# Kernel tuning notes

Measured on AMD Instinct MI355X. Metric: run time of the kernel, lower is better.

The kernel has to match this reference:

```python
import jax, jax.numpy as jnp
import numpy as np

EPS = 1e-5  # torch LayerNorm default
B, P, E, H = 16, 2048, 768, 256


def setup_inputs() -> dict:
    key = jax.random.key(0)
    k_x, k_qkv, k_lw = jax.random.split(key, 3)
    return {
        "x": jax.random.normal(k_x, (B, P, E), dtype=jnp.float32),
        "norm_w": jnp.ones((P, E), dtype=jnp.float32),
        "norm_b": jnp.zeros((P, E), dtype=jnp.float32),
        "qkv_w": jax.random.normal(k_qkv, (E, 3 * H), dtype=jnp.float32) * 0.02,
        "lin_w": jax.random.normal(k_lw, (E, H), dtype=jnp.float32) * 0.02,
        "lin_b": jnp.zeros((E,), dtype=jnp.float32),
    }


def reference(x, norm_w, norm_b, qkv_w, lin_w, lin_b):
    # LayerNorm over the last TWO dims (P, E) jointly, per batch element
    mean = jnp.mean(x, axis=(1, 2), keepdims=True)
    var = jnp.var(x, axis=(1, 2), keepdims=True)
    xn = (x - mean) * jax.lax.rsqrt(var + EPS) * norm_w + norm_b

    # QKV projection: [B,P,E] @ [E,3H] -> [B,P,3H]
    qkv = jnp.einsum("bpe,eh->bph", xn, qkv_w)
    q, k, v = jnp.split(qkv, 3, axis=2)  # each [B,P,H]

    # Unnormalized attention (no scale, no softmax)
    atten = jnp.einsum("bpd,bqd->bpq", q, k)  # [B,P,P]
    o = jnp.einsum("bpq,bqd->bpd", atten, v)  # [B,P,H]

    # Dropout p=0.0 (eval) -> identity; then Linear(H -> E) + ReLU
    out = jnp.einsum("bph,eh->bpe", o, lin_w) + lin_b
    return jax.nn.relu(out)
```

## Files before the change

kernel.cpp:

```cpp
#include <hip/hip_runtime.h>
#include <cstdint>

typedef unsigned short u16;
typedef __bf16 bf16x8 __attribute__((ext_vector_type(8)));
typedef float floatx4 __attribute__((ext_vector_type(4)));

#define BB 16
#define PP 2048
#define EE 768
#define HH 256
#define PE (PP * EE)
#define MM (BB * PP)

__device__ __forceinline__ u16 f2bf(float f) {
  union { float f; uint32_t u; } v; v.f = f;
  return (u16)((v.u + 0x7fffu + ((v.u >> 16) & 1u)) >> 16);
}

__device__ __forceinline__ void gload16(const void* g, void* l) {
  typedef __attribute__((address_space(1))) const void GV;
  typedef __attribute__((address_space(3))) void LV;
  __builtin_amdgcn_global_load_lds((GV*)g, (LV*)l, 16, 0, 0);
}

__device__ __forceinline__ int xcd_remap(int orig, int nwg) {
  return (orig & 7) * (nwg >> 3) + (orig >> 3);
}

__device__ __forceinline__ void zero_acc(floatx4 acc[4][4]) {
  const floatx4 z = {0.f, 0.f, 0.f, 0.f};
#pragma unroll
  for (int i = 0; i < 4; ++i)
#pragma unroll
    for (int j = 0; j < 4; ++j) acc[i][j] = z;
}

__device__ __forceinline__ void gemm_core(const u16* A, int lda, const u16* B, int ldb,
                                          int kIters, u16* As, u16* Bs,
                                          floatx4 acc[4][4]) {
  const int tid  = threadIdx.x;
  const int lane = tid & 63;
  const int wr   = (tid >> 7) & 1;
  const int wc   = (tid >> 6) & 1;
  const int srow = tid >> 3;
  const int scol = (tid & 7) << 3;
  const int mrow = lane & 15;
  const int kgrp = (lane >> 4) << 3;
  for (int kk = 0; kk < kIters; ++kk) {
    const u16* Ak = A + kk * 64;
    const u16* Bk = B + kk * 64;
    __syncthreads();
#pragma unroll
    for (int r = 0; r < 4; ++r) {
      gload16(Ak + (size_t)(r * 32 + srow) * lda + scol, (char*)As + r * 4096 + tid * 16);
      gload16(Bk + (size_t)(r * 32 + srow) * ldb + scol, (char*)Bs + r * 4096 + tid * 16);
    }
    __syncthreads();
#pragma unroll
    for (int kp = 0; kp < 2; ++kp) {
      const int ko = kp * 32 + kgrp;
      bf16x8 af[4], bq[4];
#pragma unroll
      for (int i = 0; i < 4; ++i) {
        af[i] = *(const bf16x8*)(As + (wr * 64 + i * 16 + mrow) * 64 + ko);
        bq[i] = *(const bf16x8*)(Bs + (wc * 64 + i * 16 + mrow) * 64 + ko);
      }
#pragma unroll
      for (int i = 0; i < 4; ++i)
#pragma unroll
        for (int j = 0; j < 4; ++j)
          acc[i][j] = __builtin_amdgcn_mfma_f32_16x16x32_bf16(af[i], bq[j], acc[i][j], 0, 0, 0);
    }
  }
}

template <typename F>
__device__ __forceinline__ void epilogue(floatx4 acc[4][4], F f) {
  const int lane = threadIdx.x & 63;
  const int wr = (threadIdx.x >> 7) & 1, wc = (threadIdx.x >> 6) & 1;
  const int r0 = (lane >> 4) * 4, c0 = lane & 15;
#pragma unroll
  for (int i = 0; i < 4; ++i)
#pragma unroll
    for (int j = 0; j < 4; ++j)
#pragma unroll
      for (int r = 0; r < 4; ++r)
        f(wr * 64 + i * 16 + r0 + r, wc * 64 + j * 16 + c0, acc[i][j][r]);
}

__global__ __launch_bounds__(256) void k_reduce1(const float* __restrict__ x,
                                                 float* __restrict__ psum,
                                                 float* __restrict__ psq) {
  const int b = blockIdx.y, blk = blockIdx.x, tid = threadIdx.x;
  const float4* xb = (const float4*)(x + (size_t)b * PE + (size_t)blk * 12288);
  float s = 0.f, q = 0.f;
#pragma unroll
  for (int i = 0; i < 12; ++i) {
    float4 v = xb[tid + i * 256];
    s += v.x + v.y + v.z + v.w;
    q += v.x * v.x + v.y * v.y + v.z * v.z + v.w * v.w;
  }
  for (int off = 32; off > 0; off >>= 1) { s += __shfl_down(s, off); q += __shfl_down(q, off); }
  __shared__ float ls[4], lq[4];
  if ((tid & 63) == 0) { ls[tid >> 6] = s; lq[tid >> 6] = q; }
  __syncthreads();
  if (tid == 0) {
    psum[b * 128 + blk] = ls[0] + ls[1] + ls[2] + ls[3];
    psq [b * 128 + blk] = lq[0] + lq[1] + lq[2] + lq[3];
  }
}

__global__ void k_reduce2(const float* __restrict__ psum, const float* __restrict__ psq,
                          float* __restrict__ stats) {
  const int b = blockIdx.x, tid = threadIdx.x;
  float s = psum[b * 128 + tid], q = psq[b * 128 + tid];
  for (int off = 32; off > 0; off >>= 1) { s += __shfl_down(s, off); q += __shfl_down(q, off); }
  __shared__ float ls[2], lq[2];
  if ((tid & 63) == 0) { ls[tid >> 6] = s; lq[tid >> 6] = q; }
  __syncthreads();
  if (tid == 0) {
    float S = ls[0] + ls[1], Q = lq[0] + lq[1];
    const float invN = 1.f / (float)PE;
    float mean = S * invN;
    float var = Q * invN - mean * mean;
    stats[b * 2] = mean;
    stats[b * 2 + 1] = rsqrtf(var + 1e-5f);
  }
}

__global__ __launch_bounds__(256) void k_ln(const float* __restrict__ x,
                                            const float* __restrict__ w,
                                            const float* __restrict__ bia,
                                            const float* __restrict__ stats,
                                            u16* __restrict__ xn) {
  const float4* x4 = (const float4*)x;
  const float4* w4 = (const float4*)w;
  const float4* b4 = (const float4*)bia;
  for (int vi = blockIdx.x * 256 + threadIdx.x; vi < (PE / 4) * BB; vi += gridDim.x * 256) {
    int bidx = vi / (PE / 4);
    int wi = vi - bidx * (PE / 4);
    float4 xv = x4[vi], wv = w4[wi], bv = b4[wi];
    float mean = stats[bidx * 2], rstd = stats[bidx * 2 + 1];
    ushort4 o;
    o.x = f2bf((xv.x - mean) * rstd * wv.x + bv.x);
    o.y = f2bf((xv.y - mean) * rstd * wv.y + bv.y);
    o.z = f2bf((xv.z - mean) * rstd * wv.z + bv.z);
    o.w = f2bf((xv.w - mean) * rstd * wv.w + bv.w);
    ((ushort4*)xn)[vi] = o;
  }
}

__global__ void k_transpose_w(const float* __restrict__ src, u16* __restrict__ dst) {
  __shared__ float t[32][33];
  const int e0 = blockIdx.x * 32, n0 = blockIdx.y * 32;
  const int tx = threadIdx.x, ty = threadIdx.y;
#pragma unroll
  for (int j = 0; j < 4; ++j)
    t[ty + j * 8][tx] = src[(size_t)(e0 + ty + j * 8) * 768 + n0 + tx];
  __syncthreads();
#pragma unroll
  for (int j = 0; j < 4; ++j)
    dst[(size_t)(n0 + ty + j * 8) * 768 + e0 + tx] = f2bf(t[tx][ty + j * 8]);
}

__global__ void k_cast(const float* __restrict__ src, u16* __restrict__ dst, int n4) {
  int i = blockIdx.x * 256 + threadIdx.x;
  if (i < n4) {
    float4 v = ((const float4*)src)[i];
    ushort4 o;
    o.x = f2bf(v.x); o.y = f2bf(v.y); o.z = f2bf(v.z); o.w = f2bf(v.w);
    ((ushort4*)dst)[i] = o;
  }
}

__global__ __launch_bounds__(256) void k_gemm_qkv(const u16* __restrict__ xn,
                                                  const u16* __restrict__ wT,
                                                  u16* __restrict__ q_buf,
                                                  u16* __restrict__ kT,
                                                  u16* __restrict__ vT) {
  __shared__ __align__(16) u16 sbuf[128 * 64 * 2];
  u16* As = sbuf;
  u16* Bs = sbuf + 128 * 64;
  floatx4 acc[4][4];
  zero_acc(acc);
  const int t = xcd_remap(blockIdx.x, 1536);
  const int xt = t % 6, yt = t / 6;
  const int tM = yt * 128, tN = xt * 128;
  gemm_core(xn + (size_t)tM * EE, EE, wT + (size_t)tN * EE, EE, 12, As, Bs, acc);

  if (xt < 2) {
    epilogue(acc, [&](int gr, int gc, float v) {
      q_buf[(size_t)(tM + gr) * HH + xt * 128 + gc] = f2bf(v);
    });
  } else {
    const int b = yt >> 4;
    const int p_base = (yt & 15) * 128;
    u16* dst = ((xt < 4) ? kT : vT) + (size_t)b * (HH * PP);
    const int dbase = (xt - ((xt < 4) ? 2 : 4)) * 128;
    u16 (*tt)[144] = (u16(*)[144])sbuf;
    const int tid = threadIdx.x;
    const int lane = tid & 63;
    const int wr = (tid >> 7) & 1, wc = (tid >> 6) & 1;
    const int r0 = (lane >> 4) * 4, c0 = lane & 15;
#pragma unroll
    for (int h = 0; h < 2; ++h) {
      __syncthreads();
      if (wc == h) {
#pragma unroll
        for (int i = 0; i < 4; ++i)
#pragma unroll
          for (int j = 0; j < 4; ++j)
#pragma unroll
            for (int r = 0; r < 4; ++r)
              tt[j * 16 + c0][wr * 64 + i * 16 + r0 + r] = f2bf(acc[i][j][r]);
      }
      __syncthreads();
#pragma unroll
      for (int pass = 0; pass < 4; ++pass) {
        const int row = pass * 16 + (tid >> 4);
        const int p8 = (tid & 15) * 8;
        const int d = dbase + h * 64 + row;
        uint4 vdat = *(const uint4*)&tt[row][p8];
        *(uint4*)&dst[(size_t)d * PP + p_base + p8] = vdat;
      }
    }
  }
}

__global__ __launch_bounds__(256) void k_gemm_w2(const u16* __restrict__ kT,
                                                 const u16* __restrict__ vT,
                                                 float* __restrict__ part) {
  __shared__ __align__(16) u16 As[128 * 64], Bs[128 * 64];
  floatx4 acc[4][4];
  zero_acc(acc);
  const int t = xcd_remap(blockIdx.x, 512);
  const int xt = t & 1, yt = (t >> 1) & 1, z = t >> 2;
  const int b = z >> 3, s = z & 7;
  const int tM = yt * 128, tN = xt * 128;
  const u16* A = kT + (size_t)b * (HH * PP) + (size_t)tM * PP + s * 256;
  const u16* B = vT + (size_t)b * (HH * PP) + (size_t)tN * PP + s * 256;
  gemm_core(A, PP, B, PP, 4, As, Bs, acc);
  float* P = part + (size_t)z * 65536;
  epilogue(acc, [&](int gr, int gc, float v) {
    P[(size_t)(tM + gr) * 256 + tN + gc] = v;
  });
}

__global__ void k_reduce_w2(const float* __restrict__ part, u16* __restrict__ W2) {
  const int idx = blockIdx.x * 256 + threadIdx.x;
  const int b = idx >> 16, i = idx & 65535;
  const float* p = part + ((size_t)b << 19) + i;
  float s = 0.f;
#pragma unroll
  for (int t = 0; t < 8; ++t) s += p[(size_t)t << 16];
  W2[idx] = f2bf(s);
}

__global__ __launch_bounds__(256) void k_gemm_m2(const u16* __restrict__ lwB,
                                                 const u16* __restrict__ W2,
                                                 u16* __restrict__ M2T) {
  __shared__ __align__(16) u16 As[128 * 64], Bs[128 * 64];
  floatx4 acc[4][4];
  zero_acc(acc);
  const int t = xcd_remap(blockIdx.x, 192);
  const int xt = t & 1, yt = (t >> 1) % 6, b = t / 12;
  const int tM = yt * 128, tN = xt * 128;
  const u16* A = lwB + (size_t)tM * HH;
  const u16* B = W2 + (size_t)b * 65536 + (size_t)tN * HH;
  gemm_core(A, HH, B, HH, 4, As, Bs, acc);
  u16* Mb = M2T + (size_t)b * (EE * HH);
  epilogue(acc, [&](int gr, int gc, float v) {
    Mb[(size_t)(tM + gr) * HH + tN + gc] = f2bf(v);
  });
}

__global__ __launch_bounds__(256) void k_gemm_out(const u16* __restrict__ q_buf,
                                                  const u16* __restrict__ M2T,
                                                  const float* __restrict__ lb,
                                                  float* __restrict__ out) {
  __shared__ __align__(16) u16 As[128 * 64], Bs[128 * 64];
  floatx4 acc[4][4];
  zero_acc(acc);
  const int t = xcd_remap(blockIdx.x, 1536);
  const int xt = t % 6, yt = (t / 6) % 16, b = t / 96;
  const int tM = yt * 128, tN = xt * 128;
  const u16* A = q_buf + (size_t)b * (PP * HH) + (size_t)tM * HH;
  const u16* B = M2T + (size_t)b * (EE * HH) + (size_t)tN * HH;
  gemm_core(A, HH, B, HH, 4, As, Bs, acc);
  float* ob = out + (size_t)b * PE;
  epilogue(acc, [&](int gr, int gc, float v) {
    ob[(size_t)(tM + gr) * EE + tN + gc] = fmaxf(v + lb[tN + gc], 0.f);
  });
}

extern "C" void kernel_launch(void* const* d_in, const int* in_sizes, int n_in,
                              void* d_out, int out_size, void* d_ws, size_t ws_size,
                              hipStream_t stream) {
  (void)in_sizes; (void)n_in; (void)out_size;
  const float* x  = (const float*)d_in[0];
  const float* nw = (const float*)d_in[1];
  const float* nb = (const float*)d_in[2];
  const float* qw = (const float*)d_in[3];
  const float* lw = (const float*)d_in[4];
  const float* lb = (const float*)d_in[5];
  float* out = (float*)d_out;
  char* ws = (char*)d_ws;

  size_t off = 0;
  auto alloc = [&](size_t bytes) { size_t o = off; off += (bytes + 255) & ~(size_t)255; return o; };
  const size_t o_psum = alloc(16 * 128 * 4);
  const size_t o_psq  = alloc(16 * 128 * 4);
  const size_t o_st   = alloc(16 * 2 * 4);
  const size_t o_qwT  = alloc((size_t)768 * 768 * 2);
  const size_t o_lwB  = alloc((size_t)768 * 256 * 2);
  const size_t o_q    = alloc((size_t)MM * HH * 2);
  const size_t o_kT   = alloc((size_t)BB * HH * PP * 2);
  const size_t o_vT   = alloc((size_t)BB * HH * PP * 2);
  const size_t o_W2   = alloc((size_t)BB * HH * HH * 2);
  const size_t o_M2T  = alloc((size_t)BB * EE * HH * 2);
  const size_t need_base = off;
  const size_t region = (size_t)MM * EE * 2;

  char* big = (ws_size >= need_base + region) ? (ws + need_base) : (char*)d_out;

  float* psum = (float*)(ws + o_psum);
  float* psq  = (float*)(ws + o_psq);
  float* st   = (float*)(ws + o_st);
  u16* qwT    = (u16*)(ws + o_qwT);
  u16* lwB    = (u16*)(ws + o_lwB);
  u16* q_buf  = (u16*)(ws + o_q);
  u16* kT     = (u16*)(ws + o_kT);
  u16* vT     = (u16*)(ws + o_vT);
  u16* W2     = (u16*)(ws + o_W2);
  u16* M2T    = (u16*)(ws + o_M2T);
  u16* xn     = (u16*)big;
  float* part = (float*)big;

  k_reduce1<<<dim3(128, 16), 256, 0, stream>>>(x, psum, psq);
  k_reduce2<<<16, 128, 0, stream>>>(psum, psq, st);
  k_ln<<<2048, 256, 0, stream>>>(x, nw, nb, st, xn);
  k_transpose_w<<<dim3(24, 24), dim3(32, 8), 0, stream>>>(qw, qwT);
  k_cast<<<192, 256, 0, stream>>>(lw, lwB, 768 * 256 / 4);
  k_gemm_qkv<<<1536, 256, 0, stream>>>(xn, qwT, q_buf, kT, vT);
  k_gemm_w2<<<512, 256, 0, stream>>>(kT, vT, part);
  k_reduce_w2<<<4096, 256, 0, stream>>>(part, W2);
  k_gemm_m2<<<192, 256, 0, stream>>>(lwB, W2, M2T);
  k_gemm_out<<<1536, 256, 0, stream>>>(q_buf, M2T, lb, out);
}
```

Before: 329.7 us.

## Fuse prologue kernels and switch small GEMMs to 64x64 single-wave tiles

Merges the partial reduction, weight transpose and weight cast into one launch. The two-stage statistics reduction becomes atomicAdd into a zeroed buffer, and k_ln now derives mean and rstd itself. The W2, M2 and output GEMMs move from 128x128 tiles on four waves to 64x64 tiles on a single wave, launched with four times as many blocks. The aim is to cut launch count and improve occupancy and load balance on the small-K GEMMs. The cost is lower per-block data reuse and more global traffic, plus float atomics that make the statistics order non-deterministic.

```diff
diff --git a/kernel.cpp b/kernel.cpp
--- a/kernel.cpp
+++ b/kernel.cpp
@@ -27,7 +27,7 @@
   return (orig & 7) * (nwg >> 3) + (orig >> 3);
 }
 
-__device__ __forceinline__ void zero_acc(floatx4 acc[4][4]) {
+__device__ __forceinline__ void zero_acc4(floatx4 acc[4][4]) {
   const floatx4 z = {0.f, 0.f, 0.f, 0.f};
 #pragma unroll
   for (int i = 0; i < 4; ++i)
@@ -74,8 +74,57 @@
   }
 }
 
+__device__ __forceinline__ void gemm64_core(const u16* A, int lda, const u16* B, int ldb,
+                                            int kIters, u16* As, u16* Bs,
+                                            floatx4 acc[4][4]) {
+  const int tid  = threadIdx.x;
+  const int srow = tid >> 3;
+  const int scol = (tid & 7) << 3;
+  const int mrow = tid & 15;
+  const int kgrp = (tid >> 4) << 3;
+  for (int kk = 0; kk < kIters; ++kk) {
+    const u16* Ak = A + kk * 64;
+    const u16* Bk = B + kk * 64;
+    __syncthreads();
+#pragma unroll
+    for (int r = 0; r < 8; ++r) {
+      gload16(Ak + (size_t)(r * 8 + srow) * lda + scol, (char*)As + r * 1024 + tid * 16);
+      gload16(Bk + (size_t)(r * 8 + srow) * ldb + scol, (char*)Bs + r * 1024 + tid * 16);
+    }
+    __syncthreads();
+#pragma unroll
+    for (int kp = 0; kp < 2; ++kp) {
+      const int ko = kp * 32 + kgrp;
+      bf16x8 af[4], bq[4];
+#pragma unroll
+      for (int i = 0; i < 4; ++i) {
+        af[i] = *(const bf16x8*)(As + (i * 16 + mrow) * 64 + ko);
+        bq[i] = *(const bf16x8*)(Bs + (i * 16 + mrow) * 64 + ko);
+      }
+#pragma unroll
+      for (int i = 0; i < 4; ++i)
+#pragma unroll
+        for (int j = 0; j < 4; ++j)
+          acc[i][j] = __builtin_amdgcn_mfma_f32_16x16x32_bf16(af[i], bq[j], acc[i][j], 0, 0, 0);
+    }
+  }
+}
+
 template <typename F>
-__device__ __forceinline__ void epilogue(floatx4 acc[4][4], F f) {
+__device__ __forceinline__ void epilogue64(floatx4 acc[4][4], F f) {
+  const int lane = threadIdx.x & 63;
+  const int r0 = (lane >> 4) * 4, c0 = lane & 15;
+#pragma unroll
+  for (int i = 0; i < 4; ++i)
+#pragma unroll
+    for (int j = 0; j < 4; ++j)
+#pragma unroll
+      for (int r = 0; r < 4; ++r)
+        f(i * 16 + r0 + r, j * 16 + c0, acc[i][j][r]);
+}
+
+template <typename F>
+__device__ __forceinline__ void epilogue4(floatx4 acc[4][4], F f) {
   const int lane = threadIdx.x & 63;
   const int wr = (threadIdx.x >> 7) & 1, wc = (threadIdx.x >> 6) & 1;
   const int r0 = (lane >> 4) * 4, c0 = lane & 15;
@@ -88,88 +137,75 @@
         f(wr * 64 + i * 16 + r0 + r, wc * 64 + j * 16 + c0, acc[i][j][r]);
 }
 
-__global__ __launch_bounds__(256) void k_reduce1(const float* __restrict__ x,
-                                                 float* __restrict__ psum,
-                                                 float* __restrict__ psq) {
-  const int b = blockIdx.y, blk = blockIdx.x, tid = threadIdx.x;
-  const float4* xb = (const float4*)(x + (size_t)b * PE + (size_t)blk * 12288);
-  float s = 0.f, q = 0.f;
-#pragma unroll
-  for (int i = 0; i < 12; ++i) {
-    float4 v = xb[tid + i * 256];
-    s += v.x + v.y + v.z + v.w;
-    q += v.x * v.x + v.y * v.y + v.z * v.z + v.w * v.w;
-  }
-  for (int off = 32; off > 0; off >>= 1) { s += __shfl_down(s, off); q += __shfl_down(q, off); }
-  __shared__ float ls[4], lq[4];
-  if ((tid & 63) == 0) { ls[tid >> 6] = s; lq[tid >> 6] = q; }
-  __syncthreads();
-  if (tid == 0) {
-    psum[b * 128 + blk] = ls[0] + ls[1] + ls[2] + ls[3];
-    psq [b * 128 + blk] = lq[0] + lq[1] + lq[2] + lq[3];
-  }
-}
-
-__global__ void k_reduce2(const float* __restrict__ psum, const float* __restrict__ psq,
-                          float* __restrict__ stats) {
-  const int b = blockIdx.x, tid = threadIdx.x;
-  float s = psum[b * 128 + tid], q = psq[b * 128 + tid];
-  for (int off = 32; off > 0; off >>= 1) { s += __shfl_down(s, off); q += __shfl_down(q, off); }
-  __shared__ float ls[2], lq[2];
-  if ((tid & 63) == 0) { ls[tid >> 6] = s; lq[tid >> 6] = q; }
-  __syncthreads();
-  if (tid == 0) {
-    float S = ls[0] + ls[1], Q = lq[0] + lq[1];
-    const float invN = 1.f / (float)PE;
-    float mean = S * invN;
-    float var = Q * invN - mean * mean;
-    stats[b * 2] = mean;
-    stats[b * 2 + 1] = rsqrtf(var + 1e-5f);
+__global__ __launch_bounds__(256) void k_r1p(const float* __restrict__ x,
+                                             float* __restrict__ st,
+                                             const float* __restrict__ qw,
+                                             u16* __restrict__ qwT,
+                                             const float* __restrict__ lw,
+                                             u16* __restrict__ lwB) {
+  const int bid = blockIdx.x, tid = threadIdx.x;
+  if (bid < 2048) {
+    const int b = bid >> 7, blk = bid & 127;
+    const float4* xb = (const float4*)(x + (size_t)b * PE + (size_t)blk * 12288);
+    float s = 0.f, q = 0.f;
+#pragma unroll
+    for (int i = 0; i < 12; ++i) {
+      float4 v = xb[tid + i * 256];
+      s += v.x + v.y + v.z + v.w;
+      q += v.x * v.x + v.y * v.y + v.z * v.z + v.w * v.w;
+    }
+    for (int off = 32; off > 0; off >>= 1) { s += __shfl_down(s, off); q += __shfl_down(q, off); }
+    __shared__ float ls[4], lq[4];
+    if ((tid & 63) == 0) { ls[tid >> 6] = s; lq[tid >> 6] = q; }
+    __syncthreads();
+    if (tid == 0) {
+      atomicAdd(&st[b * 2],     ls[0] + ls[1] + ls[2] + ls[3]);
+      atomicAdd(&st[b * 2 + 1], lq[0] + lq[1] + lq[2] + lq[3]);
+    }
+  } else if (bid < 2624) {
+    __shared__ float tsh[32][33];
+    const int pb = bid - 2048;
+    const int e0 = (pb % 24) * 32, n0 = (pb / 24) * 32;
+    const int tx = tid & 31, ty = tid >> 5;
+#pragma unroll
+    for (int j = 0; j < 4; ++j)
+      tsh[ty + j * 8][tx] = qw[(size_t)(e0 + ty + j * 8) * 768 + n0 + tx];
+    __syncthreads();
+#pragma unroll
+    for (int j = 0; j < 4; ++j)
+      qwT[(size_t)(n0 + ty + j * 8) * 768 + e0 + tx] = f2bf(tsh[tx][ty + j * 8]);
+  } else {
+    const int i = (bid - 2624) * 256 + tid;
+    if (i < 768 * 256 / 4) {
+      float4 v = ((const float4*)lw)[i];
+      ushort4 o;
+      o.x = f2bf(v.x); o.y = f2bf(v.y); o.z = f2bf(v.z); o.w = f2bf(v.w);
+      ((ushort4*)lwB)[i] = o;
+    }
   }
 }
 
 __global__ __launch_bounds__(256) void k_ln(const float* __restrict__ x,
                                             const float* __restrict__ w,
                                             const float* __restrict__ bia,
-                                            const float* __restrict__ stats,
+                                            const float* __restrict__ st,
                                             u16* __restrict__ xn) {
   const float4* x4 = (const float4*)x;
   const float4* w4 = (const float4*)w;
   const float4* b4 = (const float4*)bia;
+  const float invN = 1.f / (float)PE;
   for (int vi = blockIdx.x * 256 + threadIdx.x; vi < (PE / 4) * BB; vi += gridDim.x * 256) {
     int bidx = vi / (PE / 4);
     int wi = vi - bidx * (PE / 4);
     float4 xv = x4[vi], wv = w4[wi], bv = b4[wi];
-    float mean = stats[bidx * 2], rstd = stats[bidx * 2 + 1];
+    float mean = st[bidx * 2] * invN;
+    float rstd = rsqrtf(st[bidx * 2 + 1] * invN - mean * mean + 1e-5f);
     ushort4 o;
     o.x = f2bf((xv.x - mean) * rstd * wv.x + bv.x);
     o.y = f2bf((xv.y - mean) * rstd * wv.y + bv.y);
     o.z = f2bf((xv.z - mean) * rstd * wv.z + bv.z);
     o.w = f2bf((xv.w - mean) * rstd * wv.w + bv.w);
     ((ushort4*)xn)[vi] = o;
-  }
-}
-
-__global__ void k_transpose_w(const float* __restrict__ src, u16* __restrict__ dst) {
-  __shared__ float t[32][33];
-  const int e0 = blockIdx.x * 32, n0 = blockIdx.y * 32;
-  const int tx = threadIdx.x, ty = threadIdx.y;
-#pragma unroll
-  for (int j = 0; j < 4; ++j)
-    t[ty + j * 8][tx] = src[(size_t)(e0 + ty + j * 8) * 768 + n0 + tx];
-  __syncthreads();
-#pragma unroll
-  for (int j = 0; j < 4; ++j)
-    dst[(size_t)(n0 + ty + j * 8) * 768 + e0 + tx] = f2bf(t[tx][ty + j * 8]);
-}
-
-__global__ void k_cast(const float* __restrict__ src, u16* __restrict__ dst, int n4) {
-  int i = blockIdx.x * 256 + threadIdx.x;
-  if (i < n4) {
-    float4 v = ((const float4*)src)[i];
-    ushort4 o;
-    o.x = f2bf(v.x); o.y = f2bf(v.y); o.z = f2bf(v.z); o.w = f2bf(v.w);
-    ((ushort4*)dst)[i] = o;
   }
 }
 
@@ -182,14 +218,14 @@
   u16* As = sbuf;
   u16* Bs = sbuf + 128 * 64;
   floatx4 acc[4][4];
-  zero_acc(acc);
+  zero_acc4(acc);
   const int t = xcd_remap(blockIdx.x, 1536);
   const int xt = t % 6, yt = t / 6;
   const int tM = yt * 128, tN = xt * 128;
   gemm_core(xn + (size_t)tM * EE, EE, wT + (size_t)tN * EE, EE, 12, As, Bs, acc);
 
   if (xt < 2) {
-    epilogue(acc, [&](int gr, int gc, float v) {
+    epilogue4(acc, [&](int gr, int gc, float v) {
       q_buf[(size_t)(tM + gr) * HH + xt * 128 + gc] = f2bf(v);
     });
   } else {
@@ -197,7 +233,7 @@
     const int p_base = (yt & 15) * 128;
     u16* dst = ((xt < 4) ? kT : vT) + (size_t)b * (HH * PP);
     const int dbase = (xt - ((xt < 4) ? 2 : 4)) * 128;
-    u16 (*tt)[144] = (u16(*)[144])sbuf;
+    u16 (*tp)[144] = (u16(*)[144])sbuf;
     const int tid = threadIdx.x;
     const int lane = tid & 63;
     const int wr = (tid >> 7) & 1, wc = (tid >> 6) & 1;
@@ -212,7 +248,7 @@
           for (int j = 0; j < 4; ++j)
 #pragma unroll
             for (int r = 0; r < 4; ++r)
-              tt[j * 16 + c0][wr * 64 + i * 16 + r0 + r] = f2bf(acc[i][j][r]);
+              tp[j * 16 + c0][wr * 64 + i * 16 + r0 + r] = f2bf(acc[i][j][r]);
       }
       __syncthreads();
 #pragma unroll
@@ -220,28 +256,28 @@
         const int row = pass * 16 + (tid >> 4);
         const int p8 = (tid & 15) * 8;
         const int d = dbase + h * 64 + row;
-        uint4 vdat = *(const uint4*)&tt[row][p8];
+        uint4 vdat = *(const uint4*)&tp[row][p8];
         *(uint4*)&dst[(size_t)d * PP + p_base + p8] = vdat;
       }
     }
   }
 }
 
-__global__ __launch_bounds__(256) void k_gemm_w2(const u16* __restrict__ kT,
-                                                 const u16* __restrict__ vT,
-                                                 float* __restrict__ part) {
-  __shared__ __align__(16) u16 As[128 * 64], Bs[128 * 64];
+__global__ __launch_bounds__(64) void k_w2_64(const u16* __restrict__ kT,
+                                              const u16* __restrict__ vT,
+                                              float* __restrict__ part) {
+  __shared__ __align__(16) u16 sbuf[64 * 64 * 2];
   floatx4 acc[4][4];
-  zero_acc(acc);
-  const int t = xcd_remap(blockIdx.x, 512);
-  const int xt = t & 1, yt = (t >> 1) & 1, z = t >> 2;
+  zero_acc4(acc);
+  const int t = xcd_remap(blockIdx.x, 2048);
+  const int xt = t & 3, yt = (t >> 2) & 3, z = t >> 4;
   const int b = z >> 3, s = z & 7;
-  const int tM = yt * 128, tN = xt * 128;
+  const int tM = yt * 64, tN = xt * 64;
   const u16* A = kT + (size_t)b * (HH * PP) + (size_t)tM * PP + s * 256;
   const u16* B = vT + (size_t)b * (HH * PP) + (size_t)tN * PP + s * 256;
-  gemm_core(A, PP, B, PP, 4, As, Bs, acc);
+  gemm64_core(A, PP, B, PP, 4, sbuf, sbuf + 64 * 64, acc);
   float* P = part + (size_t)z * 65536;
-  epilogue(acc, [&](int gr, int gc, float v) {
+  epilogue64(acc, [&](int gr, int gc, float v) {
     P[(size_t)(tM + gr) * 256 + tN + gc] = v;
   });
 }
@@ -256,39 +292,39 @@
   W2[idx] = f2bf(s);
 }
 
-__global__ __launch_bounds__(256) void k_gemm_m2(const u16* __restrict__ lwB,
-                                                 const u16* __restrict__ W2,
-                                                 u16* __restrict__ M2T) {
-  __shared__ __align__(16) u16 As[128 * 64], Bs[128 * 64];
+__global__ __launch_bounds__(64) void k_m2_64(const u16* __restrict__ lwB,
+                                              const u16* __restrict__ W2,
+                                              u16* __restrict__ M2T) {
+  __shared__ __align__(16) u16 sbuf[64 * 64 * 2];
   floatx4 acc[4][4];
-  zero_acc(acc);
-  const int t = xcd_remap(blockIdx.x, 192);
-  const int xt = t & 1, yt = (t >> 1) % 6, b = t / 12;
-  const int tM = yt * 128, tN = xt * 128;
+  zero_acc4(acc);
+  const int t = xcd_remap(blockIdx.x, 768);
+  const int xt = t & 3, yt = (t >> 2) % 12, b = t / 48;
+  const int tM = yt * 64, tN = xt * 64;
   const u16* A = lwB + (size_t)tM * HH;
   const u16* B = W2 + (size_t)b * 65536 + (size_t)tN * HH;
-  gemm_core(A, HH, B, HH, 4, As, Bs, acc);
+  gemm64_core(A, HH, B, HH, 4, sbuf, sbuf + 64 * 64, acc);
   u16* Mb = M2T + (size_t)b * (EE * HH);
-  epilogue(acc, [&](int gr, int gc, float v) {
+  epilogue64(acc, [&](int gr, int gc, float v) {
     Mb[(size_t)(tM + gr) * HH + tN + gc] = f2bf(v);
   });
 }
 
-__global__ __launch_bounds__(256) void k_gemm_out(const u16* __restrict__ q_buf,
-                                                  const u16* __restrict__ M2T,
-                                                  const float* __restrict__ lb,
-                                                  float* __restrict__ out) {
-  __shared__ __align__(16) u16 As[128 * 64], Bs[128 * 64];
+__global__ __launch_bounds__(64) void k_out_64(const u16* __restrict__ q_buf,
+                                               const u16* __restrict__ M2T,
+                                               const float* __restrict__ lb,
+                                               float* __restrict__ out) {
+  __shared__ __align__(16) u16 sbuf[64 * 64 * 2];
   floatx4 acc[4][4];
-  zero_acc(acc);
-  const int t = xcd_remap(blockIdx.x, 1536);
-  const int xt = t % 6, yt = (t / 6) % 16, b = t / 96;
-  const int tM = yt * 128, tN = xt * 128;
+  zero_acc4(acc);
+  const int t = xcd_remap(blockIdx.x, 6144);
+  const int xt = t % 12, yt = (t / 12) % 32, b = t / 384;
+  const int tM = yt * 64, tN = xt * 64;
   const u16* A = q_buf + (size_t)b * (PP * HH) + (size_t)tM * HH;
   const u16* B = M2T + (size_t)b * (EE * HH) + (size_t)tN * HH;
-  gemm_core(A, HH, B, HH, 4, As, Bs, acc);
+  gemm64_core(A, HH, B, HH, 4, sbuf, sbuf + 64 * 64, acc);
   float* ob = out + (size_t)b * PE;
-  epilogue(acc, [&](int gr, int gc, float v) {
+  epilogue64(acc, [&](int gr, int gc, float v) {
     ob[(size_t)(tM + gr) * EE + tN + gc] = fmaxf(v + lb[tN + gc], 0.f);
   });
 }
@@ -308,8 +344,6 @@
 
   size_t off = 0;
   auto alloc = [&](size_t bytes) { size_t o = off; off += (bytes + 255) & ~(size_t)255; return o; };
-  const size_t o_psum = alloc(16 * 128 * 4);
-  const size_t o_psq  = alloc(16 * 128 * 4);
   const size_t o_st   = alloc(16 * 2 * 4);
   const size_t o_qwT  = alloc((size_t)768 * 768 * 2);
   const size_t o_lwB  = alloc((size_t)768 * 256 * 2);
@@ -323,8 +357,6 @@
 
   char* big = (ws_size >= need_base + region) ? (ws + need_base) : (char*)d_out;
 
-  float* psum = (float*)(ws + o_psum);
-  float* psq  = (float*)(ws + o_psq);
   float* st   = (float*)(ws + o_st);
   u16* qwT    = (u16*)(ws + o_qwT);
   u16* lwB    = (u16*)(ws + o_lwB);
@@ -336,14 +368,12 @@
   u16* xn     = (u16*)big;
   float* part = (float*)big;
 
-  k_reduce1<<<dim3(128, 16), 256, 0, stream>>>(x, psum, psq);
-  k_reduce2<<<16, 128, 0, stream>>>(psum, psq, st);
+  hipMemsetAsync(st, 0, 16 * 2 * 4, stream);
+  k_r1p<<<2816, 256, 0, stream>>>(x, st, qw, qwT, lw, lwB);
   k_ln<<<2048, 256, 0, stream>>>(x, nw, nb, st, xn);
-  k_transpose_w<<<dim3(24, 24), dim3(32, 8), 0, stream>>>(qw, qwT);
-  k_cast<<<192, 256, 0, stream>>>(lw, lwB, 768 * 256 / 4);
   k_gemm_qkv<<<1536, 256, 0, stream>>>(xn, qwT, q_buf, kT, vT);
-  k_gemm_w2<<<512, 256, 0, stream>>>(kT, vT, part);
+  k_w2_64<<<2048, 64, 0, stream>>>(kT, vT, part);
   k_reduce_w2<<<4096, 256, 0, stream>>>(part, W2);
-  k_gemm_m2<<<192, 256, 0, stream>>>(lwB, W2, M2T);
-  k_gemm_out<<<1536, 256, 0, stream>>>(q_buf, M2T, lb, out);
-}
+  k_m2_64<<<768, 64, 0, stream>>>(lwB, W2, M2T);
+  k_out_64<<<6144, 64, 0, stream>>>(q_buf, M2T, lb, out);
+}
```

Measured after the change: 351.5 us. 1.07x slower.
